# Kernel optimization log

Hardware: AMD Instinct MI355X
Metric: run time of the kernel (lower is better)

Reference implementation:

```python
import jax, jax.numpy as jnp
import numpy as np

DIM = 512
EPS = 1e-08
N_LAYERS = 3


def setup_inputs() -> dict:
    key = jax.random.key(0)
    ks = jax.random.split(key, 1 + 2 * N_LAYERS)
    B, N1 = 4, 2049  # batch, tokens (1 cls + 2048 feat)
    x = jax.random.normal(ks[0], (B, N1, DIM), dtype=jnp.float32)
    inp = {"x": x}
    s = 1.0 / np.sqrt(DIM)
    for i in range(N_LAYERS):
        inp[f"W{i}"] = jax.random.uniform(ks[1 + 2 * i], (DIM, DIM), jnp.float32, -s, s)
        inp[f"b{i}"] = jax.random.uniform(ks[2 + 2 * i], (DIM,), jnp.float32, -s, s)
    return inp


def _pgcn(x, Ws, bs):
    cls_token = x[:, 0]          # [B, D]
    feat = x[:, 1:]              # [B, N, D]
    n = jnp.linalg.norm(feat, axis=2, keepdims=True)
    feat_norm = feat / jnp.maximum(n, EPS)
    sim = jnp.einsum('bnd,bmd->bnm', feat_norm, feat_norm)  # [B, N, N]
    N = sim.shape[1]
    topk = max(int(N * 0.01), 100)
    # torch.topk(largest=False): kth-smallest value per row is the threshold
    kth_smallest = -jax.lax.top_k(-sim, topk)[0][..., -1:]  # [B, N, 1]
    adj = jnp.where(sim >= kth_smallest, sim, 0.0)
    # 3-layer GCN (skip_connection=False, eval mode -> dropout is identity)
    h = feat
    for W, b in zip(Ws, bs):
        support = jnp.einsum('bnd,de->bne', h, W) + b
        h = jax.nn.relu(jnp.einsum('bnm,bmd->bnd', adj, support))
    return jnp.concatenate([cls_token[:, None, :], h], axis=1)


def reference(x, W0, b0, W1, b1, W2, b2):
    return _pgcn(x, (W0, W1, W2), (b0, b1, b2))
```

## Files before the change

kernel.cpp:

```cpp
#include <hip/hip_runtime.h>
#include <hip/hip_bf16.h>
#include <math.h>

#define DIMV   512
#define NTOK   2048
#define NROWS  2049
#define NB     4
#define KSEL   100
#define EPSV   1e-8f

typedef __bf16 bf16x8 __attribute__((ext_vector_type(8)));
typedef float  f32x4  __attribute__((ext_vector_type(4)));

__device__ __forceinline__ unsigned short f2bf(float f) {
  unsigned int u = __float_as_uint(f);
  u += 0x7fffu + ((u >> 16) & 1u);
  return (unsigned short)(u >> 16);
}
__device__ __forceinline__ float bf2f(unsigned short s) {
  return __uint_as_float(((unsigned int)s) << 16);
}

#define GLDS16(g, l)                                                         \
  __builtin_amdgcn_global_load_lds(                                          \
      (const __attribute__((address_space(1))) void*)(unsigned long long)(g),\
      (__attribute__((address_space(3))) void*)(unsigned int)(unsigned long long)(l), \
      16, 0, 0)

__global__ __launch_bounds__(256)
void normprep_kernel(const float* __restrict__ x,
                     unsigned short* __restrict__ fhi,
                     unsigned short* __restrict__ flo,
                     unsigned short* __restrict__ featb,
                     const float* __restrict__ W0,
                     const float* __restrict__ W1,
                     const float* __restrict__ W2,
                     unsigned short* __restrict__ WT,
                     float* __restrict__ out)
{
  __shared__ float tile[32][33];
  const int bid = blockIdx.x;
  if (bid < 2048) {
    const int wave = bid * 4 + (threadIdx.x >> 6);
    const int lane = threadIdx.x & 63;
    const int b = wave / NTOK, r = wave % NTOK;
    const float* src = x + (long)(b * NROWS + 1 + r) * DIMV;
    const long rowoff = (long)(b * NTOK + r) * DIMV;
    float4 v0 = reinterpret_cast<const float4*>(src)[lane];
    float4 v1 = reinterpret_cast<const float4*>(src)[lane + 64];
    ushort4 u0, u1;
    u0.x = f2bf(v0.x); u0.y = f2bf(v0.y); u0.z = f2bf(v0.z); u0.w = f2bf(v0.w);
    u1.x = f2bf(v1.x); u1.y = f2bf(v1.y); u1.z = f2bf(v1.z); u1.w = f2bf(v1.w);
    reinterpret_cast<ushort4*>(featb + rowoff)[lane] = u0;
    reinterpret_cast<ushort4*>(featb + rowoff)[lane + 64] = u1;
    float ss = v0.x*v0.x + v0.y*v0.y + v0.z*v0.z + v0.w*v0.w
             + v1.x*v1.x + v1.y*v1.y + v1.z*v1.z + v1.w*v1.w;
    #pragma unroll
    for (int m = 1; m < 64; m <<= 1) ss += __shfl_xor(ss, m, 64);
    const float scale = 1.0f / fmaxf(sqrtf(ss), EPSV);
    float f[8] = {v0.x*scale, v0.y*scale, v0.z*scale, v0.w*scale,
                  v1.x*scale, v1.y*scale, v1.z*scale, v1.w*scale};
    ushort4 h0, h1, l0, l1;
    unsigned short hh[8], ll[8];
    #pragma unroll
    for (int i = 0; i < 8; i++) {
      hh[i] = f2bf(f[i]);
      ll[i] = f2bf(f[i] - bf2f(hh[i]));
    }
    h0.x = hh[0]; h0.y = hh[1]; h0.z = hh[2]; h0.w = hh[3];
    h1.x = hh[4]; h1.y = hh[5]; h1.z = hh[6]; h1.w = hh[7];
    l0.x = ll[0]; l0.y = ll[1]; l0.z = ll[2]; l0.w = ll[3];
    l1.x = ll[4]; l1.y = ll[5]; l1.z = ll[6]; l1.w = ll[7];
    reinterpret_cast<ushort4*>(fhi + rowoff)[lane]      = h0;
    reinterpret_cast<ushort4*>(fhi + rowoff)[lane + 64] = h1;
    reinterpret_cast<ushort4*>(flo + rowoff)[lane]      = l0;
    reinterpret_cast<ushort4*>(flo + rowoff)[lane + 64] = l1;
  } else if (bid < 2816) {
    const int idx = bid - 2048;
    const int z = idx >> 8;
    const int t2 = idx & 255;
    const int bx = t2 & 15, by = t2 >> 4;
    const float* W = (z == 0) ? W0 : (z == 1) ? W1 : W2;
    unsigned short* WTl = WT + (long)z * DIMV * DIMV;
    const int tx = threadIdx.x & 31, ty = threadIdx.x >> 5;
    #pragma unroll
    for (int s = 0; s < 32; s += 8)
      tile[ty + s][tx] = W[(long)(by * 32 + ty + s) * DIMV + bx * 32 + tx];
    __syncthreads();
    #pragma unroll
    for (int s = 0; s < 32; s += 8)
      WTl[(long)(bx * 32 + ty + s) * DIMV + by * 32 + tx] = f2bf(tile[tx][ty + s]);
  } else {
    const int cb = bid - 2816;
    const int b = cb >> 1, half = cb & 1;
    const long off = (long)b * NROWS * DIMV + half * 256 + threadIdx.x;
    out[off] = x[off];
  }
}

__global__ __launch_bounds__(256)
void sim_split_kernel(const unsigned short* __restrict__ Fhi,
                      const unsigned short* __restrict__ Flo,
                      float* __restrict__ C)
{
  __shared__ unsigned short AsH[128 * 32];
  __shared__ unsigned short AsL[128 * 32];
  __shared__ unsigned short BsH[128 * 32];
  __shared__ unsigned short BsL[128 * 32];
  const int t = threadIdx.x;
  const int l = t & 63;
  const int w = t >> 6;
  const int wr = w >> 1, wc = w & 1;
  const int zb = blockIdx.z;
  const int ti = blockIdx.x;
  int by = (int)((sqrtf(8.0f * (float)ti + 1.0f) - 1.0f) * 0.5f);
  while ((by + 1) * (by + 2) / 2 <= ti) by++;
  while (by * (by + 1) / 2 > ti) by--;
  const int bx = ti - by * (by + 1) / 2;
  const unsigned short* Ahi = Fhi + (long)zb * NTOK * DIMV;
  const unsigned short* Alo = Flo + (long)zb * NTOK * DIMV;
  const int row0 = by * 128;
  const int col0 = bx * 128;

  f32x4 acc[4][4];
  #pragma unroll
  for (int m = 0; m < 4; m++)
    #pragma unroll
    for (int n = 0; n < 4; n++) acc[m][n] = (f32x4){0.f, 0.f, 0.f, 0.f};

  const int r0 = t >> 2;
  const int r1 = 64 + (t >> 2);
  const int part = t & 3;
  const size_t base0 = (size_t)((t & 192) * 8);
  const size_t base1 = (size_t)((256 + (t & 192)) * 8);
  const int fr = l & 15, fg = l >> 4;

  for (int k0 = 0; k0 < DIMV; k0 += 32) {
    GLDS16(Ahi + (long)(row0 + r0) * DIMV + k0 + part * 8, AsH + base0);
    GLDS16(Ahi + (long)(row0 + r1) * DIMV + k0 + part * 8, AsH + base1);
    GLDS16(Alo + (long)(row0 + r0) * DIMV + k0 + part * 8, AsL + base0);
    GLDS16(Alo + (long)(row0 + r1) * DIMV + k0 + part * 8, AsL + base1);
    GLDS16(Ahi + (long)(col0 + r0) * DIMV + k0 + part * 8, BsH + base0);
    GLDS16(Ahi + (long)(col0 + r1) * DIMV + k0 + part * 8, BsH + base1);
    GLDS16(Alo + (long)(col0 + r0) * DIMV + k0 + part * 8, BsL + base0);
    GLDS16(Alo + (long)(col0 + r1) * DIMV + k0 + part * 8, BsL + base1);
    __syncthreads();

    bf16x8 ah[4], al[4], bh[4], bl[4];
    #pragma unroll
    for (int m = 0; m < 4; m++) {
      const int off = (wr * 64 + m * 16 + fr) * 32 + fg * 8;
      ah[m] = *reinterpret_cast<const bf16x8*>(&AsH[off]);
      al[m] = *reinterpret_cast<const bf16x8*>(&AsL[off]);
    }
    #pragma unroll
    for (int n = 0; n < 4; n++) {
      const int off = (wc * 64 + n * 16 + fr) * 32 + fg * 8;
      bh[n] = *reinterpret_cast<const bf16x8*>(&BsH[off]);
      bl[n] = *reinterpret_cast<const bf16x8*>(&BsL[off]);
    }
    #pragma unroll
    for (int m = 0; m < 4; m++)
      #pragma unroll
      for (int n = 0; n < 4; n++) {
        acc[m][n] = __builtin_amdgcn_mfma_f32_16x16x32_bf16(ah[m], bh[n], acc[m][n], 0, 0, 0);
        acc[m][n] = __builtin_amdgcn_mfma_f32_16x16x32_bf16(ah[m], bl[n], acc[m][n], 0, 0, 0);
        acc[m][n] = __builtin_amdgcn_mfma_f32_16x16x32_bf16(al[m], bh[n], acc[m][n], 0, 0, 0);
      }
    __syncthreads();
  }

  float* Cb = C + (long)zb * NTOK * NTOK;
  #pragma unroll
  for (int m = 0; m < 4; m++)
    #pragma unroll
    for (int r = 0; r < 4; r++) {
      const int row = row0 + wr * 64 + m * 16 + fg * 4 + r;
      #pragma unroll
      for (int n = 0; n < 4; n++) {
        const int col = col0 + wc * 64 + n * 16 + fr;
        Cb[(long)row * NTOK + col] = acc[m][n][r];
      }
    }
  if (bx != by) {
    #pragma unroll
    for (int m = 0; m < 4; m++)
      #pragma unroll
      for (int r = 0; r < 4; r++) {
        const int row = row0 + wr * 64 + m * 16 + fg * 4 + r;
        #pragma unroll
        for (int n = 0; n < 4; n++) {
          const int col = col0 + wc * 64 + n * 16 + fr;
          Cb[(long)col * NTOK + row] = acc[m][n][r];
        }
      }
  }
}

template<bool BIAS, bool RELU, bool BF16OUT>
__device__ __forceinline__
void gemm_body(const unsigned short* __restrict__ A,
               const unsigned short* __restrict__ Bt,
               const float* __restrict__ bias,
               void* __restrict__ Cv,
               int K, int lda, int ldb, int ldc,
               long sA, long sB, long sC,
               int bx, int by, int bz,
               unsigned short* As, unsigned short* Bs)
{
  const int t = threadIdx.x;
  const int l = t & 63;
  const int w = t >> 6;
  const int wr = w >> 1, wc = w & 1;
  A  += (long)bz * sA;
  Bt += (long)bz * sB;
  const int row0 = by * 128;
  const int col0 = bx * 64;

  f32x4 acc[4][2];
  #pragma unroll
  for (int m = 0; m < 4; m++)
    #pragma unroll
    for (int n = 0; n < 2; n++) acc[m][n] = (f32x4){0.f, 0.f, 0.f, 0.f};

  const int arow0 = t >> 2;
  const int arow1 = (t + 256) >> 2;
  const int apart = t & 3;
  const int brow  = t >> 2, bpart = t & 3;
  unsigned short* ldsA0 = As + (size_t)((t & 192) * 8);
  unsigned short* ldsA1 = As + (size_t)((256 + (t & 192)) * 8);
  unsigned short* ldsB  = Bs + (size_t)((t & 192) * 8);
  const int fr = l & 15, fg = l >> 4;

  const int nk = K >> 5;
  for (int kk = 0; kk < nk; ++kk) {
    const int k0 = kk << 5;
    GLDS16(A  + (long)(row0 + arow0) * lda + k0 + apart * 8, ldsA0);
    GLDS16(A  + (long)(row0 + arow1) * lda + k0 + apart * 8, ldsA1);
    GLDS16(Bt + (long)(col0 + brow)  * ldb + k0 + bpart * 8, ldsB);
    __syncthreads();

    bf16x8 af[4], bfr[2];
    #pragma unroll
    for (int m = 0; m < 4; m++)
      af[m] = *reinterpret_cast<const bf16x8*>(
          &As[(wr * 64 + m * 16 + fr) * 32 + fg * 8]);
    #pragma unroll
    for (int n = 0; n < 2; n++)
      bfr[n] = *reinterpret_cast<const bf16x8*>(
          &Bs[(wc * 32 + n * 16 + fr) * 32 + fg * 8]);
    #pragma unroll
    for (int m = 0; m < 4; m++)
      #pragma unroll
      for (int n = 0; n < 2; n++)
        acc[m][n] = __builtin_amdgcn_mfma_f32_16x16x32_bf16(af[m], bfr[n],
                                                            acc[m][n], 0, 0, 0);
    __syncthreads();
  }

  #pragma unroll
  for (int m = 0; m < 4; m++) {
    #pragma unroll
    for (int r = 0; r < 4; r++) {
      const int row = row0 + wr * 64 + m * 16 + fg * 4 + r;
      float bv = 0.f;
      if (BIAS) bv = bias[row];
      #pragma unroll
      for (int n = 0; n < 2; n++) {
        const int col = col0 + wc * 32 + n * 16 + fr;
        float v = acc[m][n][r] + bv;
        if (RELU) v = fmaxf(v, 0.f);
        if (BF16OUT)
          ((unsigned short*)Cv)[(long)bz * sC + (long)row * ldc + col] = f2bf(v);
        else
          ((float*)Cv)[(long)bz * sC + (long)row * ldc + col] = v;
      }
    }
  }
}

template<bool BIAS, bool RELU, bool BF16OUT>
__global__ __launch_bounds__(256)
void mfma_gemm(const unsigned short* __restrict__ A,
               const unsigned short* __restrict__ Bt,
               const float* __restrict__ bias,
               void* __restrict__ Cv,
               int K, int lda, int ldb, int ldc,
               long sA, long sB, long sC)
{
  __shared__ unsigned short As[128 * 32];
  __shared__ unsigned short Bs[64 * 32];
  const int nx = gridDim.x, ny = gridDim.y;
  int lin = blockIdx.x + nx * (blockIdx.y + ny * blockIdx.z);
  const int nwg = nx * ny * (int)gridDim.z;
  const int chunk = nwg >> 3;
  lin = (lin & 7) * chunk + (lin >> 3);
  const int bx = lin % nx;
  const int tmp = lin / nx;
  const int by = tmp % ny;
  const int bz = tmp / ny;
  gemm_body<BIAS, RELU, BF16OUT>(A, Bt, bias, Cv, K, lda, ldb, ldc,
                                 sA, sB, sC, bx, by, bz, As, Bs);
}

__global__ __launch_bounds__(256)
void kthgemm_kernel(const float* __restrict__ sim,
                    unsigned short* __restrict__ adjb,
                    const unsigned short* __restrict__ WT0,
                    const unsigned short* __restrict__ hb,
                    const float* __restrict__ bias0,
                    unsigned short* __restrict__ supT)
{
  __shared__ unsigned short As[128 * 32];
  __shared__ unsigned short Bs[64 * 32];
  if (blockIdx.x < 512) {
    const int bid = blockIdx.x;
    const int bx = bid & 31, by = (bid >> 5) & 3, bz = bid >> 7;
    gemm_body<true, false, true>(WT0, hb, bias0, supT,
                                 DIMV, DIMV, DIMV, NTOK,
                                 0L, (long)NTOK * DIMV, (long)DIMV * NTOK,
                                 bx, by, bz, As, Bs);
    return;
  }
  const int wid = (blockIdx.x - 512) * 4 + (threadIdx.x >> 6);
  const int lane = threadIdx.x & 63;
  const float4* row = reinterpret_cast<const float4*>(sim + (long)wid * NTOK);
  unsigned int key[32];
  #pragma unroll
  for (int i = 0; i < 8; i++) {
    const float4 v = row[lane + i * 64];
    const float f[4] = {v.x, v.y, v.z, v.w};
    #pragma unroll
    for (int j = 0; j < 4; j++) {
      const unsigned int b = __float_as_uint(f[j]);
      key[i * 4 + j] = (b & 0x80000000u) ? ~b : (b | 0x80000000u);
    }
  }
  unsigned int lo = 0x406FFFFFu, hi = 0xBF900000u;
  for (int it = 0; it < 31; ++it) {
    const unsigned int mid =
        (unsigned int)(((unsigned long long)lo + (unsigned long long)hi) >> 1);
    unsigned int total = 0;
    #pragma unroll
    for (int j = 0; j < 32; j++)
      total += (unsigned int)__popcll(__ballot(key[j] <= mid));
    if (total >= KSEL) hi = mid; else lo = mid + 1u;
  }
  ushort4* orow = reinterpret_cast<ushort4*>(adjb + (long)wid * NTOK);
  #pragma unroll
  for (int i = 0; i < 8; i++) {
    ushort4 o;
    unsigned short* op = &o.x;
    #pragma unroll
    for (int j = 0; j < 4; j++) {
      const unsigned int k = key[i * 4 + j];
      const unsigned int bits = (k & 0x80000000u) ? (k ^ 0x80000000u) : ~k;
      op[j] = (k >= lo) ? f2bf(__uint_as_float(bits)) : (unsigned short)0;
    }
    orow[lane + i * 64] = o;
  }
}

extern "C" void kernel_launch(void* const* d_in, const int* in_sizes, int n_in,
                              void* d_out, int out_size, void* d_ws, size_t ws_size,
                              hipStream_t stream) {
  const float* x  = (const float*)d_in[0];
  const float* Ws[3] = {(const float*)d_in[1], (const float*)d_in[3], (const float*)d_in[5]};
  const float* bs[3] = {(const float*)d_in[2], (const float*)d_in[4], (const float*)d_in[6]};
  float* out = (float*)d_out;

  char* ws = (char*)d_ws;
  unsigned short* fhi    = (unsigned short*)(ws);
  unsigned short* flo    = (unsigned short*)(ws + 8388608UL);
  float*          sim    = (float*)(ws + 16777216UL);
  unsigned short* adjb   = (unsigned short*)(ws + 83886080UL);
  unsigned short* supT   = (unsigned short*)(ws + 117440512UL);
  unsigned short* hb     = (unsigned short*)(ws + 125829120UL);
  unsigned short* wtb    = (unsigned short*)(ws + 134217728UL);

  normprep_kernel<<<dim3(2824), 256, 0, stream>>>(
      x, fhi, flo, hb, Ws[0], Ws[1], Ws[2], wtb, out);

  sim_split_kernel<<<dim3(136, 1, NB), 256, 0, stream>>>(fhi, flo, sim);

  kthgemm_kernel<<<dim3(2560), 256, 0, stream>>>(sim, adjb, wtb, hb, bs[0], supT);

  for (int lyr = 0; lyr < 3; lyr++) {
    if (lyr > 0) {
      mfma_gemm<true, false, true>
          <<<dim3(NTOK/64, DIMV/128, NB), 256, 0, stream>>>(
          wtb + (long)lyr * DIMV * DIMV, hb, bs[lyr], supT,
          DIMV, DIMV, DIMV, NTOK,
          0L, (long)NTOK * DIMV, (long)DIMV * NTOK);
    }
    if (lyr < 2) {
      mfma_gemm<false, true, true>
          <<<dim3(DIMV/64, NTOK/128, NB), 256, 0, stream>>>(
          adjb, supT, nullptr, hb,
          NTOK, NTOK, NTOK, DIMV,
          (long)NTOK * NTOK, (long)DIMV * NTOK, (long)NTOK * DIMV);
    } else {
      mfma_gemm<false, true, false>
          <<<dim3(DIMV/64, NTOK/128, NB), 256, 0, stream>>>(
          adjb, supT, nullptr, out + DIMV,
          NTOK, NTOK, NTOK, DIMV,
          (long)NTOK * NTOK, (long)DIMV * NTOK, (long)NROWS * DIMV);
    }
  }
}
```

Baseline: 244.4 us.

## Fuse sim GEMM, layer-0 support GEMM and top-k into persistent work-queue kernel

Replaces the separate similarity-GEMM and kth/support kernels with one persistent kernel. Blocks pull tasks from atomic queues: sim tiles first, then the layer-0 support GEMM tiles, then the top-k row tasks. Each top-k task spins on per-row-panel counters until all 16 sim tiles covering its rows have been written. The intent is to overlap the selection phase with the tail of the sim GEMM and remove a kernel boundary, at the cost of atomic traffic, spin-waiting, and dependence on correct release/acquire ordering.

```diff
diff --git a/kernel.cpp b/kernel.cpp
--- a/kernel.cpp
+++ b/kernel.cpp
@@ -26,6 +26,10 @@
       (const __attribute__((address_space(1))) void*)(unsigned long long)(g),\
       (__attribute__((address_space(3))) void*)(unsigned int)(unsigned long long)(l), \
       16, 0, 0)
+
+#define CTR_SIMQ  64
+#define CTR_G1Q   65
+#define CTR_KTHQ  66
 
 __global__ __launch_bounds__(256)
 void normprep_kernel(const float* __restrict__ x,
@@ -36,7 +40,8 @@
                      const float* __restrict__ W1,
                      const float* __restrict__ W2,
                      unsigned short* __restrict__ WT,
-                     float* __restrict__ out)
+                     float* __restrict__ out,
+                     int* __restrict__ ctrs)
 {
   __shared__ float tile[32][33];
   const int bid = blockIdx.x;
@@ -92,31 +97,32 @@
       WTl[(long)(bx * 32 + ty + s) * DIMV + by * 32 + tx] = f2bf(tile[tx][ty + s]);
   } else {
     const int cb = bid - 2816;
+    if (cb == 0 && threadIdx.x < 80) ctrs[threadIdx.x] = 0;
     const int b = cb >> 1, half = cb & 1;
     const long off = (long)b * NROWS * DIMV + half * 256 + threadIdx.x;
     out[off] = x[off];
   }
 }
 
-__global__ __launch_bounds__(256)
-void sim_split_kernel(const unsigned short* __restrict__ Fhi,
-                      const unsigned short* __restrict__ Flo,
-                      float* __restrict__ C)
-{
-  __shared__ unsigned short AsH[128 * 32];
-  __shared__ unsigned short AsL[128 * 32];
-  __shared__ unsigned short BsH[128 * 32];
-  __shared__ unsigned short BsL[128 * 32];
+__device__ void sim_tile_task(int task, const unsigned short* __restrict__ Fhi,
+                              const unsigned short* __restrict__ Flo,
+                              float* __restrict__ C, char* lds,
+                              int* __restrict__ ctrs)
+{
+  unsigned short* AsH = (unsigned short*)lds;
+  unsigned short* AsL = AsH + 4096;
+  unsigned short* BsH = AsL + 4096;
+  unsigned short* BsL = BsH + 4096;
   const int t = threadIdx.x;
   const int l = t & 63;
   const int w = t >> 6;
   const int wr = w >> 1, wc = w & 1;
-  const int zb = blockIdx.z;
-  const int ti = blockIdx.x;
-  int by = (int)((sqrtf(8.0f * (float)ti + 1.0f) - 1.0f) * 0.5f);
-  while ((by + 1) * (by + 2) / 2 <= ti) by++;
-  while (by * (by + 1) / 2 > ti) by--;
-  const int bx = ti - by * (by + 1) / 2;
+  const int zb = task & 3;
+  int q = task >> 2;
+  int c = 0, cum = 0;
+  while (cum + (16 - c) <= q) { cum += 16 - c; ++c; }
+  const int bx = c;
+  const int by = c + (q - cum);
   const unsigned short* Ahi = Fhi + (long)zb * NTOK * DIMV;
   const unsigned short* Alo = Flo + (long)zb * NTOK * DIMV;
   const int row0 = by * 128;
@@ -194,6 +200,14 @@
           Cb[(long)col * NTOK + row] = acc[m][n][r];
         }
       }
+  }
+  __syncthreads();
+  if (threadIdx.x == 0) {
+    __hip_atomic_fetch_add(&ctrs[zb * 16 + by], 1,
+                           __ATOMIC_RELEASE, __HIP_MEMORY_SCOPE_AGENT);
+    if (bx != by)
+      __hip_atomic_fetch_add(&ctrs[zb * 16 + bx], 1,
+                             __ATOMIC_RELEASE, __HIP_MEMORY_SCOPE_AGENT);
   }
 }
 
@@ -279,6 +293,107 @@
   }
 }
 
+__device__ void kth_task(int task, const float* __restrict__ sim,
+                         unsigned short* __restrict__ adjb,
+                         int* __restrict__ ctrs)
+{
+  const int zb = task & 3;
+  const int q = task >> 2;
+  const int p = q >> 5;
+  const int rg = q & 31;
+  if (threadIdx.x == 0) {
+    while (__hip_atomic_load(&ctrs[zb * 16 + p],
+                             __ATOMIC_ACQUIRE, __HIP_MEMORY_SCOPE_AGENT) < 16)
+      __builtin_amdgcn_s_sleep(2);
+  }
+  __syncthreads();
+  const long rowidx = (long)zb * NTOK + p * 128 + rg * 4 + (threadIdx.x >> 6);
+  const int lane = threadIdx.x & 63;
+  const float4* row = reinterpret_cast<const float4*>(sim + rowidx * NTOK);
+  unsigned int key[32];
+  #pragma unroll
+  for (int i = 0; i < 8; i++) {
+    const float4 v = row[lane + i * 64];
+    const float f[4] = {v.x, v.y, v.z, v.w};
+    #pragma unroll
+    for (int j = 0; j < 4; j++) {
+      const unsigned int b = __float_as_uint(f[j]);
+      key[i * 4 + j] = (b & 0x80000000u) ? ~b : (b | 0x80000000u);
+    }
+  }
+  unsigned int lo = 0x406FFFFFu, hi = 0xBF900000u;
+  for (int it = 0; it < 31; ++it) {
+    const unsigned int mid =
+        (unsigned int)(((unsigned long long)lo + (unsigned long long)hi) >> 1);
+    unsigned int total = 0;
+    #pragma unroll
+    for (int j = 0; j < 32; j++)
+      total += (unsigned int)__popcll(__ballot(key[j] <= mid));
+    if (total >= KSEL) hi = mid; else lo = mid + 1u;
+  }
+  ushort4* orow = reinterpret_cast<ushort4*>(adjb + rowidx * NTOK);
+  #pragma unroll
+  for (int i = 0; i < 8; i++) {
+    ushort4 o;
+    unsigned short* op = &o.x;
+    #pragma unroll
+    for (int j = 0; j < 4; j++) {
+      const unsigned int k = key[i * 4 + j];
+      const unsigned int bits = (k & 0x80000000u) ? (k ^ 0x80000000u) : ~k;
+      op[j] = (k >= lo) ? f2bf(__uint_as_float(bits)) : (unsigned short)0;
+    }
+    orow[lane + i * 64] = o;
+  }
+}
+
+__global__ __launch_bounds__(256)
+void mega_kernel(const unsigned short* __restrict__ fhi,
+                 const unsigned short* __restrict__ flo,
+                 float* __restrict__ sim,
+                 unsigned short* __restrict__ adjb,
+                 const unsigned short* __restrict__ WT0,
+                 const unsigned short* __restrict__ hb,
+                 const float* __restrict__ bias0,
+                 unsigned short* __restrict__ supT,
+                 int* __restrict__ ctrs)
+{
+  __shared__ char lds[32768];
+  int* tsh = (int*)lds;
+  for (;;) {
+    __syncthreads();
+    if (threadIdx.x == 0) tsh[0] = atomicAdd(&ctrs[CTR_SIMQ], 1);
+    __syncthreads();
+    const int t = tsh[0];
+    __syncthreads();
+    if (t >= 544) break;
+    sim_tile_task(t, fhi, flo, sim, lds, ctrs);
+  }
+  for (;;) {
+    __syncthreads();
+    if (threadIdx.x == 0) tsh[0] = atomicAdd(&ctrs[CTR_G1Q], 1);
+    __syncthreads();
+    const int t = tsh[0];
+    __syncthreads();
+    if (t >= 512) break;
+    const int bx = t & 31, by = (t >> 5) & 3, bz = t >> 7;
+    gemm_body<true, false, true>(WT0, hb, bias0, supT,
+                                 DIMV, DIMV, DIMV, NTOK,
+                                 0L, (long)NTOK * DIMV, (long)DIMV * NTOK,
+                                 bx, by, bz,
+                                 (unsigned short*)lds,
+                                 (unsigned short*)(lds + 16384));
+  }
+  for (;;) {
+    __syncthreads();
+    if (threadIdx.x == 0) tsh[0] = atomicAdd(&ctrs[CTR_KTHQ], 1);
+    __syncthreads();
+    const int t = tsh[0];
+    __syncthreads();
+    if (t >= 2048) return;
+    kth_task(t, sim, adjb, ctrs);
+  }
+}
+
 template<bool BIAS, bool RELU, bool BF16OUT>
 __global__ __launch_bounds__(256)
 void mfma_gemm(const unsigned short* __restrict__ A,
@@ -303,64 +418,6 @@
                                  sA, sB, sC, bx, by, bz, As, Bs);
 }
 
-__global__ __launch_bounds__(256)
-void kthgemm_kernel(const float* __restrict__ sim,
-                    unsigned short* __restrict__ adjb,
-                    const unsigned short* __restrict__ WT0,
-                    const unsigned short* __restrict__ hb,
-                    const float* __restrict__ bias0,
-                    unsigned short* __restrict__ supT)
-{
-  __shared__ unsigned short As[128 * 32];
-  __shared__ unsigned short Bs[64 * 32];
-  if (blockIdx.x < 512) {
-    const int bid = blockIdx.x;
-    const int bx = bid & 31, by = (bid >> 5) & 3, bz = bid >> 7;
-    gemm_body<true, false, true>(WT0, hb, bias0, supT,
-                                 DIMV, DIMV, DIMV, NTOK,
-                                 0L, (long)NTOK * DIMV, (long)DIMV * NTOK,
-                                 bx, by, bz, As, Bs);
-    return;
-  }
-  const int wid = (blockIdx.x - 512) * 4 + (threadIdx.x >> 6);
-  const int lane = threadIdx.x & 63;
-  const float4* row = reinterpret_cast<const float4*>(sim + (long)wid * NTOK);
-  unsigned int key[32];
-  #pragma unroll
-  for (int i = 0; i < 8; i++) {
-    const float4 v = row[lane + i * 64];
-    const float f[4] = {v.x, v.y, v.z, v.w};
-    #pragma unroll
-    for (int j = 0; j < 4; j++) {
-      const unsigned int b = __float_as_uint(f[j]);
-      key[i * 4 + j] = (b & 0x80000000u) ? ~b : (b | 0x80000000u);
-    }
-  }
-  unsigned int lo = 0x406FFFFFu, hi = 0xBF900000u;
-  for (int it = 0; it < 31; ++it) {
-    const unsigned int mid =
-        (unsigned int)(((unsigned long long)lo + (unsigned long long)hi) >> 1);
-    unsigned int total = 0;
-    #pragma unroll
-    for (int j = 0; j < 32; j++)
-      total += (unsigned int)__popcll(__ballot(key[j] <= mid));
-    if (total >= KSEL) hi = mid; else lo = mid + 1u;
-  }
-  ushort4* orow = reinterpret_cast<ushort4*>(adjb + (long)wid * NTOK);
-  #pragma unroll
-  for (int i = 0; i < 8; i++) {
-    ushort4 o;
-    unsigned short* op = &o.x;
-    #pragma unroll
-    for (int j = 0; j < 4; j++) {
-      const unsigned int k = key[i * 4 + j];
-      const unsigned int bits = (k & 0x80000000u) ? (k ^ 0x80000000u) : ~k;
-      op[j] = (k >= lo) ? f2bf(__uint_as_float(bits)) : (unsigned short)0;
-    }
-    orow[lane + i * 64] = o;
-  }
-}
-
 extern "C" void kernel_launch(void* const* d_in, const int* in_sizes, int n_in,
                               void* d_out, int out_size, void* d_ws, size_t ws_size,
                               hipStream_t stream) {
@@ -377,13 +434,13 @@
   unsigned short* supT   = (unsigned short*)(ws + 117440512UL);
   unsigned short* hb     = (unsigned short*)(ws + 125829120UL);
   unsigned short* wtb    = (unsigned short*)(ws + 134217728UL);
+  int*            ctrs   = (int*)(ws + 135790592UL);
 
   normprep_kernel<<<dim3(2824), 256, 0, stream>>>(
-      x, fhi, flo, hb, Ws[0], Ws[1], Ws[2], wtb, out);
-
-  sim_split_kernel<<<dim3(136, 1, NB), 256, 0, stream>>>(fhi, flo, sim);
-
-  kthgemm_kernel<<<dim3(2560), 256, 0, stream>>>(sim, adjb, wtb, hb, bs[0], supT);
+      x, fhi, flo, hb, Ws[0], Ws[1], Ws[2], wtb, out, ctrs);
+
+  mega_kernel<<<dim3(1280), 256, 0, stream>>>(
+      fhi, flo, sim, adjb, wtb, hb, bs[0], supT, ctrs);
 
   for (int lyr = 0; lyr < 3; lyr++) {
     if (lyr > 0) {
```

After: 317.9 us. 30.1% more time.

## Co-schedule layer-0 support GEMM with sim GEMM, split out kth selection

Applied to the files above, without the earlier changes.

Moves the layer-0 support GEMM (W0·h) out of the kth-selection kernel and into the similarity GEMM launch as extra blocks, so its 512 blocks fill the idle CUs left by the 544-block triangular sim grid. The top-k threshold search becomes its own kernel. Its ballot/popcount loop is regrouped into batches of eight to expose more independent work. The shared LDS buffer is sized at 32 KB for both roles, which may change occupancy for the GEMM blocks.

```diff
diff --git a/kernel.cpp b/kernel.cpp
--- a/kernel.cpp
+++ b/kernel.cpp
@@ -98,105 +98,6 @@
   }
 }
 
-__global__ __launch_bounds__(256)
-void sim_split_kernel(const unsigned short* __restrict__ Fhi,
-                      const unsigned short* __restrict__ Flo,
-                      float* __restrict__ C)
-{
-  __shared__ unsigned short AsH[128 * 32];
-  __shared__ unsigned short AsL[128 * 32];
-  __shared__ unsigned short BsH[128 * 32];
-  __shared__ unsigned short BsL[128 * 32];
-  const int t = threadIdx.x;
-  const int l = t & 63;
-  const int w = t >> 6;
-  const int wr = w >> 1, wc = w & 1;
-  const int zb = blockIdx.z;
-  const int ti = blockIdx.x;
-  int by = (int)((sqrtf(8.0f * (float)ti + 1.0f) - 1.0f) * 0.5f);
-  while ((by + 1) * (by + 2) / 2 <= ti) by++;
-  while (by * (by + 1) / 2 > ti) by--;
-  const int bx = ti - by * (by + 1) / 2;
-  const unsigned short* Ahi = Fhi + (long)zb * NTOK * DIMV;
-  const unsigned short* Alo = Flo + (long)zb * NTOK * DIMV;
-  const int row0 = by * 128;
-  const int col0 = bx * 128;
-
-  f32x4 acc[4][4];
-  #pragma unroll
-  for (int m = 0; m < 4; m++)
-    #pragma unroll
-    for (int n = 0; n < 4; n++) acc[m][n] = (f32x4){0.f, 0.f, 0.f, 0.f};
-
-  const int r0 = t >> 2;
-  const int r1 = 64 + (t >> 2);
-  const int part = t & 3;
-  const size_t base0 = (size_t)((t & 192) * 8);
-  const size_t base1 = (size_t)((256 + (t & 192)) * 8);
-  const int fr = l & 15, fg = l >> 4;
-
-  for (int k0 = 0; k0 < DIMV; k0 += 32) {
-    GLDS16(Ahi + (long)(row0 + r0) * DIMV + k0 + part * 8, AsH + base0);
-    GLDS16(Ahi + (long)(row0 + r1) * DIMV + k0 + part * 8, AsH + base1);
-    GLDS16(Alo + (long)(row0 + r0) * DIMV + k0 + part * 8, AsL + base0);
-    GLDS16(Alo + (long)(row0 + r1) * DIMV + k0 + part * 8, AsL + base1);
-    GLDS16(Ahi + (long)(col0 + r0) * DIMV + k0 + part * 8, BsH + base0);
-    GLDS16(Ahi + (long)(col0 + r1) * DIMV + k0 + part * 8, BsH + base1);
-    GLDS16(Alo + (long)(col0 + r0) * DIMV + k0 + part * 8, BsL + base0);
-    GLDS16(Alo + (long)(col0 + r1) * DIMV + k0 + part * 8, BsL + base1);
-    __syncthreads();
-
-    bf16x8 ah[4], al[4], bh[4], bl[4];
-    #pragma unroll
-    for (int m = 0; m < 4; m++) {
-      const int off = (wr * 64 + m * 16 + fr) * 32 + fg * 8;
-      ah[m] = *reinterpret_cast<const bf16x8*>(&AsH[off]);
-      al[m] = *reinterpret_cast<const bf16x8*>(&AsL[off]);
-    }
-    #pragma unroll
-    for (int n = 0; n < 4; n++) {
-      const int off = (wc * 64 + n * 16 + fr) * 32 + fg * 8;
-      bh[n] = *reinterpret_cast<const bf16x8*>(&BsH[off]);
-      bl[n] = *reinterpret_cast<const bf16x8*>(&BsL[off]);
-    }
-    #pragma unroll
-    for (int m = 0; m < 4; m++)
-      #pragma unroll
-      for (int n = 0; n < 4; n++) {
-        acc[m][n] = __builtin_amdgcn_mfma_f32_16x16x32_bf16(ah[m], bh[n], acc[m][n], 0, 0, 0);
-        acc[m][n] = __builtin_amdgcn_mfma_f32_16x16x32_bf16(ah[m], bl[n], acc[m][n], 0, 0, 0);
-        acc[m][n] = __builtin_amdgcn_mfma_f32_16x16x32_bf16(al[m], bh[n], acc[m][n], 0, 0, 0);
-      }
-    __syncthreads();
-  }
-
-  float* Cb = C + (long)zb * NTOK * NTOK;
-  #pragma unroll
-  for (int m = 0; m < 4; m++)
-    #pragma unroll
-    for (int r = 0; r < 4; r++) {
-      const int row = row0 + wr * 64 + m * 16 + fg * 4 + r;
-      #pragma unroll
-      for (int n = 0; n < 4; n++) {
-        const int col = col0 + wc * 64 + n * 16 + fr;
-        Cb[(long)row * NTOK + col] = acc[m][n][r];
-      }
-    }
-  if (bx != by) {
-    #pragma unroll
-    for (int m = 0; m < 4; m++)
-      #pragma unroll
-      for (int r = 0; r < 4; r++) {
-        const int row = row0 + wr * 64 + m * 16 + fg * 4 + r;
-        #pragma unroll
-        for (int n = 0; n < 4; n++) {
-          const int col = col0 + wc * 64 + n * 16 + fr;
-          Cb[(long)col * NTOK + row] = acc[m][n][r];
-        }
-      }
-  }
-}
-
 template<bool BIAS, bool RELU, bool BF16OUT>
 __device__ __forceinline__
 void gemm_body(const unsigned short* __restrict__ A,
@@ -276,6 +177,175 @@
           ((float*)Cv)[(long)bz * sC + (long)row * ldc + col] = v;
       }
     }
+  }
+}
+
+__global__ __launch_bounds__(256)
+void simg1_kernel(const unsigned short* __restrict__ Fhi,
+                  const unsigned short* __restrict__ Flo,
+                  float* __restrict__ C,
+                  const unsigned short* __restrict__ WT0,
+                  const unsigned short* __restrict__ hb,
+                  const float* __restrict__ bias0,
+                  unsigned short* __restrict__ supT)
+{
+  __shared__ char lds[32768];
+  if (blockIdx.x >= 544) {
+    const int idx = blockIdx.x - 544;
+    const int bx = idx & 31, by = (idx >> 5) & 3, bz = idx >> 7;
+    gemm_body<true, false, true>(WT0, hb, bias0, supT,
+                                 DIMV, DIMV, DIMV, NTOK,
+                                 0L, (long)NTOK * DIMV, (long)DIMV * NTOK,
+                                 bx, by, bz,
+                                 (unsigned short*)lds,
+                                 (unsigned short*)(lds + 16384));
+    return;
+  }
+  unsigned short* AsH = (unsigned short*)lds;
+  unsigned short* AsL = AsH + 4096;
+  unsigned short* BsH = AsL + 4096;
+  unsigned short* BsL = BsH + 4096;
+  const int t = threadIdx.x;
+  const int l = t & 63;
+  const int w = t >> 6;
+  const int wr = w >> 1, wc = w & 1;
+  const int zb = blockIdx.x / 136;
+  const int ti = blockIdx.x - zb * 136;
+  int by = (int)((sqrtf(8.0f * (float)ti + 1.0f) - 1.0f) * 0.5f);
+  while ((by + 1) * (by + 2) / 2 <= ti) by++;
+  while (by * (by + 1) / 2 > ti) by--;
+  const int bx = ti - by * (by + 1) / 2;
+  const unsigned short* Ahi = Fhi + (long)zb * NTOK * DIMV;
+  const unsigned short* Alo = Flo + (long)zb * NTOK * DIMV;
+  const int row0 = by * 128;
+  const int col0 = bx * 128;
+
+  f32x4 acc[4][4];
+  #pragma unroll
+  for (int m = 0; m < 4; m++)
+    #pragma unroll
+    for (int n = 0; n < 4; n++) acc[m][n] = (f32x4){0.f, 0.f, 0.f, 0.f};
+
+  const int r0 = t >> 2;
+  const int r1 = 64 + (t >> 2);
+  const int part = t & 3;
+  const size_t base0 = (size_t)((t & 192) * 8);
+  const size_t base1 = (size_t)((256 + (t & 192)) * 8);
+  const int fr = l & 15, fg = l >> 4;
+
+  for (int k0 = 0; k0 < DIMV; k0 += 32) {
+    GLDS16(Ahi + (long)(row0 + r0) * DIMV + k0 + part * 8, AsH + base0);
+    GLDS16(Ahi + (long)(row0 + r1) * DIMV + k0 + part * 8, AsH + base1);
+    GLDS16(Alo + (long)(row0 + r0) * DIMV + k0 + part * 8, AsL + base0);
+    GLDS16(Alo + (long)(row0 + r1) * DIMV + k0 + part * 8, AsL + base1);
+    GLDS16(Ahi + (long)(col0 + r0) * DIMV + k0 + part * 8, BsH + base0);
+    GLDS16(Ahi + (long)(col0 + r1) * DIMV + k0 + part * 8, BsH + base1);
+    GLDS16(Alo + (long)(col0 + r0) * DIMV + k0 + part * 8, BsL + base0);
+    GLDS16(Alo + (long)(col0 + r1) * DIMV + k0 + part * 8, BsL + base1);
+    __syncthreads();
+
+    bf16x8 ah[4], al[4], bh[4], bl[4];
+    #pragma unroll
+    for (int m = 0; m < 4; m++) {
+      const int off = (wr * 64 + m * 16 + fr) * 32 + fg * 8;
+      ah[m] = *reinterpret_cast<const bf16x8*>(&AsH[off]);
+      al[m] = *reinterpret_cast<const bf16x8*>(&AsL[off]);
+    }
+    #pragma unroll
+    for (int n = 0; n < 4; n++) {
+      const int off = (wc * 64 + n * 16 + fr) * 32 + fg * 8;
+      bh[n] = *reinterpret_cast<const bf16x8*>(&BsH[off]);
+      bl[n] = *reinterpret_cast<const bf16x8*>(&BsL[off]);
+    }
+    #pragma unroll
+    for (int m = 0; m < 4; m++)
+      #pragma unroll
+      for (int n = 0; n < 4; n++) {
+        acc[m][n] = __builtin_amdgcn_mfma_f32_16x16x32_bf16(ah[m], bh[n], acc[m][n], 0, 0, 0);
+        acc[m][n] = __builtin_amdgcn_mfma_f32_16x16x32_bf16(ah[m], bl[n], acc[m][n], 0, 0, 0);
+        acc[m][n] = __builtin_amdgcn_mfma_f32_16x16x32_bf16(al[m], bh[n], acc[m][n], 0, 0, 0);
+      }
+    __syncthreads();
+  }
+
+  float* Cb = C + (long)zb * NTOK * NTOK;
+  #pragma unroll
+  for (int m = 0; m < 4; m++)
+    #pragma unroll
+    for (int r = 0; r < 4; r++) {
+      const int row = row0 + wr * 64 + m * 16 + fg * 4 + r;
+      #pragma unroll
+      for (int n = 0; n < 4; n++) {
+        const int col = col0 + wc * 64 + n * 16 + fr;
+        Cb[(long)row * NTOK + col] = acc[m][n][r];
+      }
+    }
+  if (bx != by) {
+    #pragma unroll
+    for (int m = 0; m < 4; m++)
+      #pragma unroll
+      for (int r = 0; r < 4; r++) {
+        const int row = row0 + wr * 64 + m * 16 + fg * 4 + r;
+        #pragma unroll
+        for (int n = 0; n < 4; n++) {
+          const int col = col0 + wc * 64 + n * 16 + fr;
+          Cb[(long)col * NTOK + row] = acc[m][n][r];
+        }
+      }
+  }
+}
+
+__global__ __launch_bounds__(256)
+void kth_kernel(const float* __restrict__ sim,
+                unsigned short* __restrict__ adjb)
+{
+  const long rid = (long)blockIdx.x * 4 + (threadIdx.x >> 6);
+  const int lane = threadIdx.x & 63;
+  const float4* row = reinterpret_cast<const float4*>(sim + rid * NTOK);
+  unsigned int key[32];
+  #pragma unroll
+  for (int i = 0; i < 8; i++) {
+    const float4 v = row[lane + i * 64];
+    const float f[4] = {v.x, v.y, v.z, v.w};
+    #pragma unroll
+    for (int j = 0; j < 4; j++) {
+      const unsigned int b = __float_as_uint(f[j]);
+      key[i * 4 + j] = (b & 0x80000000u) ? ~b : (b | 0x80000000u);
+    }
+  }
+  unsigned int lo = 0x406FFFFFu, hi = 0xBF900000u;
+  for (int it = 0; it < 31; ++it) {
+    const unsigned int mid =
+        (unsigned int)(((unsigned long long)lo + (unsigned long long)hi) >> 1);
+    unsigned int total = 0;
+    #pragma unroll
+    for (int c = 0; c < 4; ++c) {
+      const unsigned long long m0 = __ballot(key[c * 8 + 0] <= mid);
+      const unsigned long long m1 = __ballot(key[c * 8 + 1] <= mid);
+      const unsigned long long m2 = __ballot(key[c * 8 + 2] <= mid);
+      const unsigned long long m3 = __ballot(key[c * 8 + 3] <= mid);
+      const unsigned long long m4 = __ballot(key[c * 8 + 4] <= mid);
+      const unsigned long long m5 = __ballot(key[c * 8 + 5] <= mid);
+      const unsigned long long m6 = __ballot(key[c * 8 + 6] <= mid);
+      const unsigned long long m7 = __ballot(key[c * 8 + 7] <= mid);
+      total += (unsigned int)(__popcll(m0) + __popcll(m1) + __popcll(m2) +
+                              __popcll(m3) + __popcll(m4) + __popcll(m5) +
+                              __popcll(m6) + __popcll(m7));
+    }
+    if (total >= KSEL) hi = mid; else lo = mid + 1u;
+  }
+  ushort4* orow = reinterpret_cast<ushort4*>(adjb + rid * NTOK);
+  #pragma unroll
+  for (int i = 0; i < 8; i++) {
+    ushort4 o;
+    unsigned short* op = &o.x;
+    #pragma unroll
+    for (int j = 0; j < 4; j++) {
+      const unsigned int k = key[i * 4 + j];
+      const unsigned int bits = (k & 0x80000000u) ? (k ^ 0x80000000u) : ~k;
+      op[j] = (k >= lo) ? f2bf(__uint_as_float(bits)) : (unsigned short)0;
+    }
+    orow[lane + i * 64] = o;
   }
 }
 
@@ -303,64 +373,6 @@
                                  sA, sB, sC, bx, by, bz, As, Bs);
 }
 
-__global__ __launch_bounds__(256)
-void kthgemm_kernel(const float* __restrict__ sim,
-                    unsigned short* __restrict__ adjb,
-                    const unsigned short* __restrict__ WT0,
-                    const unsigned short* __restrict__ hb,
-                    const float* __restrict__ bias0,
-                    unsigned short* __restrict__ supT)
-{
-  __shared__ unsigned short As[128 * 32];
-  __shared__ unsigned short Bs[64 * 32];
-  if (blockIdx.x < 512) {
-    const int bid = blockIdx.x;
-    const int bx = bid & 31, by = (bid >> 5) & 3, bz = bid >> 7;
-    gemm_body<true, false, true>(WT0, hb, bias0, supT,
-                                 DIMV, DIMV, DIMV, NTOK,
-                                 0L, (long)NTOK * DIMV, (long)DIMV * NTOK,
-                                 bx, by, bz, As, Bs);
-    return;
-  }
-  const int wid = (blockIdx.x - 512) * 4 + (threadIdx.x >> 6);
-  const int lane = threadIdx.x & 63;
-  const float4* row = reinterpret_cast<const float4*>(sim + (long)wid * NTOK);
-  unsigned int key[32];
-  #pragma unroll
-  for (int i = 0; i < 8; i++) {
-    const float4 v = row[lane + i * 64];
-    const float f[4] = {v.x, v.y, v.z, v.w};
-    #pragma unroll
-    for (int j = 0; j < 4; j++) {
-      const unsigned int b = __float_as_uint(f[j]);
-      key[i * 4 + j] = (b & 0x80000000u) ? ~b : (b | 0x80000000u);
-    }
-  }
-  unsigned int lo = 0x406FFFFFu, hi = 0xBF900000u;
-  for (int it = 0; it < 31; ++it) {
-    const unsigned int mid =
-        (unsigned int)(((unsigned long long)lo + (unsigned long long)hi) >> 1);
-    unsigned int total = 0;
-    #pragma unroll
-    for (int j = 0; j < 32; j++)
-      total += (unsigned int)__popcll(__ballot(key[j] <= mid));
-    if (total >= KSEL) hi = mid; else lo = mid + 1u;
-  }
-  ushort4* orow = reinterpret_cast<ushort4*>(adjb + (long)wid * NTOK);
-  #pragma unroll
-  for (int i = 0; i < 8; i++) {
-    ushort4 o;
-    unsigned short* op = &o.x;
-    #pragma unroll
-    for (int j = 0; j < 4; j++) {
-      const unsigned int k = key[i * 4 + j];
-      const unsigned int bits = (k & 0x80000000u) ? (k ^ 0x80000000u) : ~k;
-      op[j] = (k >= lo) ? f2bf(__uint_as_float(bits)) : (unsigned short)0;
-    }
-    orow[lane + i * 64] = o;
-  }
-}
-
 extern "C" void kernel_launch(void* const* d_in, const int* in_sizes, int n_in,
                               void* d_out, int out_size, void* d_ws, size_t ws_size,
                               hipStream_t stream) {
@@ -381,9 +393,10 @@
   normprep_kernel<<<dim3(2824), 256, 0, stream>>>(
       x, fhi, flo, hb, Ws[0], Ws[1], Ws[2], wtb, out);
 
-  sim_split_kernel<<<dim3(136, 1, NB), 256, 0, stream>>>(fhi, flo, sim);
-
-  kthgemm_kernel<<<dim3(2560), 256, 0, stream>>>(sim, adjb, wtb, hb, bs[0], supT);
+  simg1_kernel<<<dim3(1056), 256, 0, stream>>>(
+      fhi, flo, sim, wtb, hb, bs[0], supT);
+
+  kth_kernel<<<dim3(2048), 256, 0, stream>>>(sim, adjb);
 
   for (int lyr = 0; lyr < 3; lyr++) {
     if (lyr > 0) {
```

After: 242.4 us. About the same (-0.8%).
